# Kernel tuning notes

Hardware: AMD Instinct MI355X
Metric: run time of the kernel (lower is better)

Reference implementation:

```python
import jax, jax.numpy as jnp
import numpy as np

GROUPS = 32
EPS = 1e-5


def setup_inputs() -> dict:
    key = jax.random.key(0)
    ks = jax.random.split(key, 6)
    B, H, W, C = 4, 64, 64, 512
    s = 1.0 / np.sqrt(C)
    return {
        "x": jax.random.normal(ks[0], (B, H, W, C), dtype=jnp.float32),
        "gamma": jnp.ones((C,), jnp.float32),
        "beta": jnp.zeros((C,), jnp.float32),
        "wq": jax.random.normal(ks[1], (C, C), jnp.float32) * s,
        "bq": jnp.zeros((C,), jnp.float32),
        "wk": jax.random.normal(ks[2], (C, C), jnp.float32) * s,
        "bk": jnp.zeros((C,), jnp.float32),
        "wv": jax.random.normal(ks[3], (C, C), jnp.float32) * s,
        "bv": jnp.zeros((C,), jnp.float32),
        "wp": jax.random.normal(ks[4], (C, C), jnp.float32) * s,
        "bp": jnp.zeros((C,), jnp.float32),
    }


def _group_norm(x, gamma, beta):
    B, H, W, C = x.shape
    cg = C // GROUPS
    xg = x.reshape(B, H, W, GROUPS, cg)
    mu = jnp.mean(xg, axis=(1, 2, 4), keepdims=True)
    var = jnp.var(xg, axis=(1, 2, 4), keepdims=True)
    xn = ((xg - mu) * jax.lax.rsqrt(var + EPS)).reshape(B, H, W, C)
    return xn * gamma + beta


def reference(x, gamma, beta, wq, bq, wk, bk, wv, bv, wp, bp):
    B, H, W, C = x.shape
    N = H * W
    xn = _group_norm(x, gamma, beta)
    # 1x1 convs == channel-wise dense layers
    q = (xn @ wq + bq).reshape(B, N, C)
    k = (xn @ wk + bk).reshape(B, N, C)
    v = (xn @ wv + bv).reshape(B, N, C)
    scores = jnp.einsum("bic,bjc->bij", q, k) * (C ** -0.5)  # [B, N, N]
    attn = jax.nn.softmax(scores, axis=-1)
    out = jnp.einsum("bij,bjc->bic", attn, v).reshape(B, H, W, C)
    return out @ wp + bp + x
```

## Files before the change

### kernel.cpp

```cpp
#include <hip/hip_runtime.h>
#include <hip/hip_bf16.h>

typedef __attribute__((ext_vector_type(4))) float f32x4;
typedef __attribute__((ext_vector_type(8))) short s16x8;
typedef unsigned short ushort_t;

#define N_DIM 4096
#define C_DIM 512

static __device__ __forceinline__ unsigned short f2bf(float f) {
    union { float f; unsigned u; } v; v.f = f;
    unsigned r = v.u + 0x7FFFu + ((v.u >> 16) & 1u);
    return (unsigned short)(r >> 16);
}
static __device__ __forceinline__ float bf2f(unsigned short u) {
    union { unsigned u; float f; } v; v.u = ((unsigned)u) << 16;
    return v.f;
}

__global__ void gn_stats_kernel(const float* __restrict__ x, float* __restrict__ stats) {
    int bg = blockIdx.x;
    int b = bg >> 5, g = bg & 31;
    const float* base = x + (size_t)b * (N_DIM * C_DIM) + g * 16;
    float sum = 0.f, ss = 0.f;
    for (int n = threadIdx.x; n < N_DIM; n += 256) {
        const float4* p = (const float4*)(base + (size_t)n * C_DIM);
        #pragma unroll
        for (int t = 0; t < 4; ++t) {
            float4 v = p[t];
            sum += v.x + v.y + v.z + v.w;
            ss  += v.x*v.x + v.y*v.y + v.z*v.z + v.w*v.w;
        }
    }
    #pragma unroll
    for (int o = 32; o > 0; o >>= 1) {
        sum += __shfl_down(sum, o);
        ss  += __shfl_down(ss, o);
    }
    __shared__ float red[8];
    int wid = threadIdx.x >> 6, lane = threadIdx.x & 63;
    if (lane == 0) { red[wid*2] = sum; red[wid*2+1] = ss; }
    __syncthreads();
    if (threadIdx.x == 0) {
        sum = red[0]+red[2]+red[4]+red[6];
        ss  = red[1]+red[3]+red[5]+red[7];
        float mean = sum * (1.f/65536.f);
        float var  = ss  * (1.f/65536.f) - mean*mean;
        stats[bg*2]   = mean;
        stats[bg*2+1] = rsqrtf(var + 1e-5f);
    }
}

__global__ void gn_norm_kernel(const float* __restrict__ x, const float* __restrict__ gamma,
                               const float* __restrict__ beta, const float* __restrict__ stats,
                               ushort_t* __restrict__ xn) {
    size_t i = ((size_t)blockIdx.x * 256 + threadIdx.x) * 4;
    int c = (int)(i & 511);
    int b = (int)(i >> 21);
    int bg = b*32 + (c >> 4);
    float mean = stats[bg*2], rstd = stats[bg*2+1];
    float4 v  = *(const float4*)(x + i);
    float4 ga = *(const float4*)(gamma + c);
    float4 be = *(const float4*)(beta + c);
    ushort4 o;
    o.x = f2bf((v.x - mean) * rstd * ga.x + be.x);
    o.y = f2bf((v.y - mean) * rstd * ga.y + be.y);
    o.z = f2bf((v.z - mean) * rstd * ga.z + be.z);
    o.w = f2bf((v.w - mean) * rstd * ga.w + be.w);
    *(ushort4*)(xn + i) = o;
}

__global__ void wconv_kernel(const float* __restrict__ wq, const float* __restrict__ wk,
                             const float* __restrict__ wv, const float* __restrict__ wp,
                             ushort_t* __restrict__ wt) {
    int idx = blockIdx.x * 256 + threadIdx.x;
    int m = idx >> 18;
    int r = idx & 262143;
    int ci = r >> 9, co = r & 511;
    const float* w = (m == 0) ? wq : (m == 1) ? wk : (m == 2) ? wv : wp;
    wt[(size_t)m * 262144 + (size_t)co * 512 + ci] = f2bf(w[(size_t)ci * 512 + co]);
}

__global__ __launch_bounds__(256) void qkv_kernel(const ushort_t* __restrict__ xn, const ushort_t* __restrict__ wt,
                         const float* __restrict__ bq, const float* __restrict__ bk, const float* __restrict__ bv,
                         ushort_t* __restrict__ q, ushort_t* __restrict__ k, ushort_t* __restrict__ v) {
    __shared__ char alds[2][8192];
    __shared__ char blds[2][8192];
    const int tid = threadIdx.x;
    const int w = tid >> 6, lane = tid & 63;
    const int lr = lane & 15, lg = lane >> 4;
    const int wr = w >> 1, wc = w & 1;
    const int m0 = blockIdx.x * 128;
    const int c0g = blockIdx.y * 128;
    const int z = c0g >> 9;
    const int c0 = c0g & 511;
    const ushort_t* W = wt + (size_t)z * 262144;
    const float* bias = (z == 0) ? bq : (z == 1) ? bk : bv;
    const float scale = (z == 0) ? 0.04419417382415922f : 1.0f;

    f32x4 acc[4][4];
    #pragma unroll
    for (int a = 0; a < 4; ++a)
        #pragma unroll
        for (int b = 0; b < 4; ++b) acc[a][b] = (f32x4){0.f,0.f,0.f,0.f};

    const int g1 = tid, g2 = tid + 256;
    const int r1 = g1 >> 2, s1 = ((g1 & 3) ^ (r1 & 3)) << 4;
    const int r2g = g2 >> 2, s2 = ((g2 & 3) ^ (r2g & 3)) << 4;

    auto STAGE = [&](int buf, int k0) {
        const char* A = (const char*)xn + (size_t)(m0) * 1024 + k0 * 2;
        const char* B = (const char*)W + (size_t)(c0) * 1024 + k0 * 2;
        __builtin_amdgcn_global_load_lds((const __attribute__((address_space(1))) void*)(A + (size_t)r1 * 1024 + s1),
            (__attribute__((address_space(3))) void*)(&alds[buf][g1 * 16]), 16, 0, 0);
        __builtin_amdgcn_global_load_lds((const __attribute__((address_space(1))) void*)(A + (size_t)r2g * 1024 + s2),
            (__attribute__((address_space(3))) void*)(&alds[buf][g2 * 16]), 16, 0, 0);
        __builtin_amdgcn_global_load_lds((const __attribute__((address_space(1))) void*)(B + (size_t)r1 * 1024 + s1),
            (__attribute__((address_space(3))) void*)(&blds[buf][g1 * 16]), 16, 0, 0);
        __builtin_amdgcn_global_load_lds((const __attribute__((address_space(1))) void*)(B + (size_t)r2g * 1024 + s2),
            (__attribute__((address_space(3))) void*)(&blds[buf][g2 * 16]), 16, 0, 0);
    };

    STAGE(0, 0);
    for (int ks = 0; ks < 16; ++ks) {
        const int cur = ks & 1;
        if (ks < 15) {
            STAGE(cur ^ 1, (ks + 1) * 32);
            asm volatile("s_waitcnt vmcnt(4)" ::: "memory");
        } else {
            asm volatile("s_waitcnt vmcnt(0)" ::: "memory");
        }
        __builtin_amdgcn_s_barrier();
        asm volatile("" ::: "memory");
        s16x8 af[4], bf[4];
        #pragma unroll
        for (int mi = 0; mi < 4; ++mi) {
            int row = wr * 64 + mi * 16 + lr;
            af[mi] = *(const s16x8*)(&alds[cur][row * 64 + ((lg ^ (lr & 3)) << 4)]);
        }
        #pragma unroll
        for (int ni = 0; ni < 4; ++ni) {
            int row = wc * 64 + ni * 16 + lr;
            bf[ni] = *(const s16x8*)(&blds[cur][row * 64 + ((lg ^ (lr & 3)) << 4)]);
        }
        #pragma unroll
        for (int mi = 0; mi < 4; ++mi)
            #pragma unroll
            for (int ni = 0; ni < 4; ++ni)
                acc[mi][ni] = __builtin_amdgcn_mfma_f32_16x16x32_bf16(af[mi], bf[ni], acc[mi][ni], 0, 0, 0);
        asm volatile("" ::: "memory");
        __builtin_amdgcn_s_barrier();
    }

    if (z < 2) {
        ushort_t* out = (z == 0) ? q : k;
        #pragma unroll
        for (int ni = 0; ni < 4; ++ni) {
            int cg = c0 + wc * 64 + ni * 16 + lr;
            float bb = bias[cg];
            #pragma unroll
            for (int mi = 0; mi < 4; ++mi) {
                int row = m0 + wr * 64 + mi * 16 + lg * 4;
                #pragma unroll
                for (int r2 = 0; r2 < 4; ++r2)
                    out[(size_t)(row + r2) * 512 + cg] = f2bf((acc[mi][ni][r2] + bb) * scale);
            }
        }
    } else {
        #pragma unroll
        for (int ni = 0; ni < 4; ++ni) {
            int cg = c0 + wc * 64 + ni * 16 + lr;
            float bb = bias[cg];
            #pragma unroll
            for (int mi = 0; mi < 4; ++mi) {
                int row = m0 + wr * 64 + mi * 16 + lg * 4;
                int batch = row >> 12, j = row & 4095;
                ushort4 o;
                o.x = f2bf(acc[mi][ni][0] + bb);
                o.y = f2bf(acc[mi][ni][1] + bb);
                o.z = f2bf(acc[mi][ni][2] + bb);
                o.w = f2bf(acc[mi][ni][3] + bb);
                *(ushort4*)(v + (size_t)batch * (512*4096) + (size_t)cg * 4096 + j) = o;
            }
        }
    }
}

__global__ __launch_bounds__(256) void attn_kernel(const ushort_t* __restrict__ q, const ushort_t* __restrict__ k,
                          const ushort_t* __restrict__ vt, ushort_t* __restrict__ Op0,
                          ushort_t* __restrict__ Op1, float2* __restrict__ stats2) {
    __shared__ char slds[131072 + 8192 + 512];
    char* plds = slds + 131072;
    float* rlds = (float*)(slds + 131072 + 8192);
    const int tid = threadIdx.x;
    const int w = tid >> 6, lane = tid & 63;
    const int lr = lane & 15, lg = lane >> 4;
    const int batch = blockIdx.y;
    const int js = blockIdx.z;
    const int i0 = blockIdx.x * 64;
    const int jbase = js * 2048;
    const char* kb = (const char*)(k  + (size_t)batch * (4096 * 512));
    const char* vb = (const char*)(vt + (size_t)batch * (512 * 4096));
    const ushort_t* qb = q + (size_t)batch * (4096 * 512);

    s16x8 qf[16];
    {
        const ushort_t* qrow = qb + (size_t)(i0 + w * 16 + lr) * 512 + lg * 8;
        #pragma unroll
        for (int t = 0; t < 16; ++t) qf[t] = *(const s16x8*)(qrow + t * 32);
    }

    f32x4 acc[8][4];
    #pragma unroll
    for (int a = 0; a < 8; ++a)
        #pragma unroll
        for (int b = 0; b < 4; ++b) acc[a][b] = (f32x4){0.f,0.f,0.f,0.f};
    float m = -1e30f, s = 0.f;

    const int vswz = ((lane & 3) ^ ((lane >> 3) & 3)) << 4;

    auto STAGE_K = [&](int buf, int j0) {
        char* lb = slds + buf * 65536;
        const char* gk = kb + (size_t)j0 * 1024;
        #pragma unroll
        for (int r = 0; r < 8; ++r) {
            int row = w * 8 + r;
            __builtin_amdgcn_global_load_lds(
                (const __attribute__((address_space(1))) void*)(gk + (size_t)row * 1024 + ((lane ^ r) << 4)),
                (__attribute__((address_space(3))) void*)(lb + row * 1024), 16, 0, 0);
        }
    };
    auto STAGE_V = [&](int buf, int j0) {
        char* lv = slds + buf * 65536 + 32768;
        const char* gv = vb + (size_t)j0 * 2;
        #pragma unroll
        for (int r = 0; r < 8; ++r) {
            int p = w * 8 + r;
            int c = p * 16 + (lane >> 2);
            __builtin_amdgcn_global_load_lds(
                (const __attribute__((address_space(1))) void*)(gv + (size_t)c * 8192 + vswz),
                (__attribute__((address_space(3))) void*)(lv + p * 1024), 16, 0, 0);
        }
    };

    auto QKSM = [&](int buf, int pbuf) {
        const char* kl = slds + buf * 65536;
        f32x4 sa = {0,0,0,0}, sb = {0,0,0,0}, sc2 = {0,0,0,0}, sd = {0,0,0,0};
        #pragma unroll
        for (int tt = 0; tt < 16; tt += 2) {
            s16x8 k0f = *(const s16x8*)(kl + lr * 1024        + ((tt*64 + lg*16)     ^ ((lr&7)*16)));
            s16x8 k1f = *(const s16x8*)(kl + lr * 1024        + (((tt+1)*64 + lg*16) ^ ((lr&7)*16)));
            s16x8 k2f = *(const s16x8*)(kl + (16+lr) * 1024   + ((tt*64 + lg*16)     ^ ((lr&7)*16)));
            s16x8 k3f = *(const s16x8*)(kl + (16+lr) * 1024   + (((tt+1)*64 + lg*16) ^ ((lr&7)*16)));
            sa  = __builtin_amdgcn_mfma_f32_16x16x32_bf16(k0f, qf[tt],   sa,  0,0,0);
            sb  = __builtin_amdgcn_mfma_f32_16x16x32_bf16(k1f, qf[tt+1], sb,  0,0,0);
            sc2 = __builtin_amdgcn_mfma_f32_16x16x32_bf16(k2f, qf[tt],   sc2, 0,0,0);
            sd  = __builtin_amdgcn_mfma_f32_16x16x32_bf16(k3f, qf[tt+1], sd,  0,0,0);
        }
        f32x4 s1 = sa + sb;
        f32x4 s2 = sc2 + sd;

        float tm = fmaxf(fmaxf(fmaxf(s1[0], s1[1]), fmaxf(s1[2], s1[3])),
                         fmaxf(fmaxf(s2[0], s2[1]), fmaxf(s2[2], s2[3])));
        tm = fmaxf(tm, __shfl_xor(tm, 16));
        tm = fmaxf(tm, __shfl_xor(tm, 32));
        float resc = 1.f;
        if (!__all(tm <= m + 8.f)) {
            float mnew = fmaxf(m, tm);
            resc = __expf(m - mnew);
            s *= resc;
            m = mnew;
        }
        f32x4 p1, p2;
        #pragma unroll
        for (int r2 = 0; r2 < 4; ++r2) { p1[r2] = __expf(s1[r2] - m); p2[r2] = __expf(s2[r2] - m); }
        float ts = p1[0]+p1[1]+p1[2]+p1[3] + p2[0]+p2[1]+p2[2]+p2[3];
        ts += __shfl_xor(ts, 16);
        ts += __shfl_xor(ts, 32);
        s += ts;

        unsigned w0 = (unsigned)f2bf(p1[0]) | ((unsigned)f2bf(p1[1]) << 16);
        unsigned w1 = (unsigned)f2bf(p1[2]) | ((unsigned)f2bf(p1[3]) << 16);
        unsigned w2 = (unsigned)f2bf(p2[0]) | ((unsigned)f2bf(p2[1]) << 16);
        unsigned w3 = (unsigned)f2bf(p2[2]) | ((unsigned)f2bf(p2[3]) << 16);
        char* prow = plds + pbuf * 4096 + w * 1024 + lr * 64 + ((lg & 1) << 3);
        *(uint2*)(prow + ((((lg >> 1)    ) ^ (lr & 3)) << 4)) = (uint2){w0, w1};
        *(uint2*)(prow + (((2 | (lg >> 1)) ^ (lr & 3)) << 4)) = (uint2){w2, w3};
        if (lg == 0) rlds[pbuf * 64 + w * 16 + lr] = resc;
    };

    STAGE_K(0, jbase);
    STAGE_V(0, jbase);
    STAGE_K(1, jbase + 32);
    asm volatile("s_waitcnt vmcnt(8)" ::: "memory");
    __builtin_amdgcn_s_barrier();
    asm volatile("" ::: "memory");
    QKSM(0, 0);
    asm volatile("s_waitcnt lgkmcnt(0)" ::: "memory");
    __builtin_amdgcn_s_barrier();
    asm volatile("" ::: "memory");

    for (int t = 0; t < 64; ++t) {
        const int cur = t & 1, nxt = cur ^ 1;
        if (t < 62) STAGE_K(cur, jbase + (t + 2) * 32);
        if (t < 63) STAGE_V(nxt, jbase + (t + 1) * 32);

        {
            const float* rr = rlds + cur * 64;
            float rf0 = rr[lr], rf1 = rr[16 + lr], rf2 = rr[32 + lr], rf3 = rr[48 + lr];
            if (__any(rf0 != 1.f || rf1 != 1.f || rf2 != 1.f || rf3 != 1.f)) {
                #pragma unroll
                for (int ct = 0; ct < 8; ++ct) {
                    acc[ct][0] *= rf0; acc[ct][1] *= rf1; acc[ct][2] *= rf2; acc[ct][3] *= rf3;
                }
            }
        }
        s16x8 pf[4];
        #pragma unroll
        for (int g = 0; g < 4; ++g)
            pf[g] = *(const s16x8*)(plds + cur * 4096 + g * 1024 + lr * 64 + ((lg ^ (lr & 3)) << 4));

        const char* vl = slds + cur * 65536 + 32768;
        #pragma unroll
        for (int ct = 0; ct < 8; ++ct) {
            int c = w * 128 + ct * 16 + lr;
            s16x8 vf = *(const s16x8*)(vl + c * 64 + ((lg ^ ((lr >> 1) & 3)) << 4));
            #pragma unroll
            for (int g = 0; g < 4; ++g)
                acc[ct][g] = __builtin_amdgcn_mfma_f32_16x16x32_bf16(vf, pf[g], acc[ct][g], 0,0,0);
        }

        if (t < 63) QKSM(nxt, nxt);

        asm volatile("s_waitcnt vmcnt(0) lgkmcnt(0)" ::: "memory");
        __builtin_amdgcn_s_barrier();
        asm volatile("" ::: "memory");
    }

    if (lg == 0) {
        rlds[w * 16 + lr] = 1.f / s;
        stats2[((size_t)(batch * 2 + js)) * 4096 + i0 + w * 16 + lr] = (float2){m, s};
    }
    __syncthreads();
    ushort_t* Op = js ? Op1 : Op0;
    float inv0 = rlds[lr], inv1 = rlds[16 + lr], inv2 = rlds[32 + lr], inv3 = rlds[48 + lr];
    #pragma unroll
    for (int ct = 0; ct < 8; ++ct) {
        #pragma unroll
        for (int g = 0; g < 4; ++g) {
            float iv = (g == 0) ? inv0 : (g == 1) ? inv1 : (g == 2) ? inv2 : inv3;
            ushort4 o;
            o.x = f2bf(acc[ct][g][0] * iv);
            o.y = f2bf(acc[ct][g][1] * iv);
            o.z = f2bf(acc[ct][g][2] * iv);
            o.w = f2bf(acc[ct][g][3] * iv);
            *(ushort4*)(Op + ((size_t)batch * 4096 + i0 + g*16 + lr) * 512
                        + w * 128 + ct * 16 + lg * 4) = o;
        }
    }
}

__global__ void combine_kernel(ushort_t* __restrict__ Op0, const ushort_t* __restrict__ Op1,
                               const float2* __restrict__ stats2) {
    int idx = blockIdx.x * 256 + threadIdx.x;
    int row = idx >> 7;
    int cc = (idx & 127) << 2;
    int b = row >> 12, r = row & 4095;
    float2 st0 = stats2[((size_t)(b * 2 + 0)) * 4096 + r];
    float2 st1 = stats2[((size_t)(b * 2 + 1)) * 4096 + r];
    float M = fmaxf(st0.x, st1.x);
    float w0 = __expf(st0.x - M) * st0.y;
    float w1 = __expf(st1.x - M) * st1.y;
    float rden = 1.f / (w0 + w1);
    w0 *= rden; w1 *= rden;
    size_t off = (size_t)row * 512 + cc;
    ushort4 a = *(ushort4*)(Op0 + off);
    ushort4 c4 = *(const ushort4*)(Op1 + off);
    ushort4 o;
    o.x = f2bf(w0 * bf2f(a.x) + w1 * bf2f(c4.x));
    o.y = f2bf(w0 * bf2f(a.y) + w1 * bf2f(c4.y));
    o.z = f2bf(w0 * bf2f(a.z) + w1 * bf2f(c4.z));
    o.w = f2bf(w0 * bf2f(a.w) + w1 * bf2f(c4.w));
    *(ushort4*)(Op0 + off) = o;
}

__global__ __launch_bounds__(256) void proj_kernel(const ushort_t* __restrict__ O, const ushort_t* __restrict__ wt,
                          const float* __restrict__ bp, const float* __restrict__ x, float* __restrict__ out) {
    __shared__ char alds[2][8192];
    __shared__ char blds[2][8192];
    const int tid = threadIdx.x;
    const int w = tid >> 6, lane = tid & 63;
    const int lr = lane & 15, lg = lane >> 4;
    const int wr = w >> 1, wc = w & 1;
    const int m0 = blockIdx.x * 128;
    const int c0 = blockIdx.y * 128;
    const ushort_t* W = wt + (size_t)3 * 262144;

    f32x4 acc[4][4];
    #pragma unroll
    for (int a = 0; a < 4; ++a)
        #pragma unroll
        for (int b = 0; b < 4; ++b) acc[a][b] = (f32x4){0.f,0.f,0.f,0.f};

    const int g1 = tid, g2 = tid + 256;
    const int r1 = g1 >> 2, s1 = ((g1 & 3) ^ (r1 & 3)) << 4;
    const int r2g = g2 >> 2, s2 = ((g2 & 3) ^ (r2g & 3)) << 4;

    auto STAGE = [&](int buf, int k0) {
        const char* A = (const char*)O + (size_t)(m0) * 1024 + k0 * 2;
        const char* B = (const char*)W + (size_t)(c0) * 1024 + k0 * 2;
        __builtin_amdgcn_global_load_lds((const __attribute__((address_space(1))) void*)(A + (size_t)r1 * 1024 + s1),
            (__attribute__((address_space(3))) void*)(&alds[buf][g1 * 16]), 16, 0, 0);
        __builtin_amdgcn_global_load_lds((const __attribute__((address_space(1))) void*)(A + (size_t)r2g * 1024 + s2),
            (__attribute__((address_space(3))) void*)(&alds[buf][g2 * 16]), 16, 0, 0);
        __builtin_amdgcn_global_load_lds((const __attribute__((address_space(1))) void*)(B + (size_t)r1 * 1024 + s1),
            (__attribute__((address_space(3))) void*)(&blds[buf][g1 * 16]), 16, 0, 0);
        __builtin_amdgcn_global_load_lds((const __attribute__((address_space(1))) void*)(B + (size_t)r2g * 1024 + s2),
            (__attribute__((address_space(3))) void*)(&blds[buf][g2 * 16]), 16, 0, 0);
    };

    STAGE(0, 0);
    for (int ks = 0; ks < 16; ++ks) {
        const int cur = ks & 1;
        if (ks < 15) {
            STAGE(cur ^ 1, (ks + 1) * 32);
            asm volatile("s_waitcnt vmcnt(4)" ::: "memory");
        } else {
            asm volatile("s_waitcnt vmcnt(0)" ::: "memory");
        }
        __builtin_amdgcn_s_barrier();
        asm volatile("" ::: "memory");
        s16x8 af[4], bf[4];
        #pragma unroll
        for (int mi = 0; mi < 4; ++mi) {
            int row = wr * 64 + mi * 16 + lr;
            af[mi] = *(const s16x8*)(&alds[cur][row * 64 + ((lg ^ (lr & 3)) << 4)]);
        }
        #pragma unroll
        for (int ni = 0; ni < 4; ++ni) {
            int row = wc * 64 + ni * 16 + lr;
            bf[ni] = *(const s16x8*)(&blds[cur][row * 64 + ((lg ^ (lr & 3)) << 4)]);
        }
        #pragma unroll
        for (int mi = 0; mi < 4; ++mi)
            #pragma unroll
            for (int ni = 0; ni < 4; ++ni)
                acc[mi][ni] = __builtin_amdgcn_mfma_f32_16x16x32_bf16(af[mi], bf[ni], acc[mi][ni], 0, 0, 0);
        asm volatile("" ::: "memory");
        __builtin_amdgcn_s_barrier();
    }

    #pragma unroll
    for (int ni = 0; ni < 4; ++ni) {
        int cg = c0 + wc * 64 + ni * 16 + lr;
        float bb = bp[cg];
        #pragma unroll
        for (int mi = 0; mi < 4; ++mi) {
            int row = m0 + wr * 64 + mi * 16 + lg * 4;
            #pragma unroll
            for (int r2 = 0; r2 < 4; ++r2) {
                size_t idx = (size_t)(row + r2) * 512 + cg;
                out[idx] = acc[mi][ni][r2] + bb + x[idx];
            }
        }
    }
}

extern "C" void kernel_launch(void* const* d_in, const int* in_sizes, int n_in,
                              void* d_out, int out_size, void* d_ws, size_t ws_size,
                              hipStream_t stream) {
    (void)in_sizes; (void)n_in; (void)out_size; (void)ws_size;
    const float* x     = (const float*)d_in[0];
    const float* gamma = (const float*)d_in[1];
    const float* beta  = (const float*)d_in[2];
    const float* wq    = (const float*)d_in[3];
    const float* bq    = (const float*)d_in[4];
    const float* wk    = (const float*)d_in[5];
    const float* bk    = (const float*)d_in[6];
    const float* wv    = (const float*)d_in[7];
    const float* bv    = (const float*)d_in[8];
    const float* wp    = (const float*)d_in[9];
    const float* bp    = (const float*)d_in[10];
    float* out = (float*)d_out;

    char* ws = (char*)d_ws;
    ushort_t* wt    = (ushort_t*)(ws);
    float*    stats = (float*)(ws + (2ull<<20));
    float2*   st2   = (float2*)(ws + (3ull<<20));
    ushort_t* xn    = (ushort_t*)(ws + (4ull<<20));
    ushort_t* qb    = (ushort_t*)(ws + (20ull<<20));
    ushort_t* kb    = (ushort_t*)(ws + (36ull<<20));
    ushort_t* vt    = (ushort_t*)(ws + (52ull<<20));
    ushort_t* Ob    = (ushort_t*)(ws + (68ull<<20));

    hipLaunchKernelGGL(wconv_kernel,    dim3(4096),       dim3(256), 0, stream, wq, wk, wv, wp, wt);
    hipLaunchKernelGGL(gn_stats_kernel, dim3(128),        dim3(256), 0, stream, x, stats);
    hipLaunchKernelGGL(gn_norm_kernel,  dim3(8192),       dim3(256), 0, stream, x, gamma, beta, stats, xn);
    hipLaunchKernelGGL(qkv_kernel,      dim3(128, 12),    dim3(256), 0, stream, xn, wt, bq, bk, bv, qb, kb, vt);
    hipLaunchKernelGGL(attn_kernel,     dim3(64, 4, 2),   dim3(256), 0, stream, qb, kb, vt, Ob, xn, st2);
    hipLaunchKernelGGL(combine_kernel,  dim3(8192),       dim3(256), 0, stream, Ob, xn, st2);
    hipLaunchKernelGGL(proj_kernel,     dim3(128, 4),     dim3(256), 0, stream, Ob, wt, bp, x, out);
}
```

Baseline: 359.1 us.

## Drop split-KV attention and combine kernel; reorder QK softmax ahead of PV

The attention kernel no longer splits the key/value range across two blocks. Each block now walks all 4096 keys, and the separate combine kernel with its partial outputs and per-row stats is removed. This removes an extra launch and the write and re-read of two partial output tensors. The cost is half as many blocks (256 instead of 512), so each block carries a longer serial loop. The next tile's QK/softmax is also moved ahead of the current tile's PV MFMAs to change how instructions interleave, and the prologue wait now drains all outstanding loads.

```diff
diff --git a/kernel.cpp b/kernel.cpp
--- a/kernel.cpp
+++ b/kernel.cpp
@@ -12,10 +12,6 @@
     union { float f; unsigned u; } v; v.f = f;
     unsigned r = v.u + 0x7FFFu + ((v.u >> 16) & 1u);
     return (unsigned short)(r >> 16);
-}
-static __device__ __forceinline__ float bf2f(unsigned short u) {
-    union { unsigned u; float f; } v; v.u = ((unsigned)u) << 16;
-    return v.f;
 }
 
 __global__ void gn_stats_kernel(const float* __restrict__ x, float* __restrict__ stats) {
@@ -187,8 +183,7 @@
 }
 
 __global__ __launch_bounds__(256) void attn_kernel(const ushort_t* __restrict__ q, const ushort_t* __restrict__ k,
-                          const ushort_t* __restrict__ vt, ushort_t* __restrict__ Op0,
-                          ushort_t* __restrict__ Op1, float2* __restrict__ stats2) {
+                          const ushort_t* __restrict__ vt, ushort_t* __restrict__ O) {
     __shared__ char slds[131072 + 8192 + 512];
     char* plds = slds + 131072;
     float* rlds = (float*)(slds + 131072 + 8192);
@@ -196,9 +191,7 @@
     const int w = tid >> 6, lane = tid & 63;
     const int lr = lane & 15, lg = lane >> 4;
     const int batch = blockIdx.y;
-    const int js = blockIdx.z;
     const int i0 = blockIdx.x * 64;
-    const int jbase = js * 2048;
     const char* kb = (const char*)(k  + (size_t)batch * (4096 * 512));
     const char* vb = (const char*)(vt + (size_t)batch * (512 * 4096));
     const ushort_t* qb = q + (size_t)batch * (4096 * 512);
@@ -289,10 +282,10 @@
         if (lg == 0) rlds[pbuf * 64 + w * 16 + lr] = resc;
     };
 
-    STAGE_K(0, jbase);
-    STAGE_V(0, jbase);
-    STAGE_K(1, jbase + 32);
-    asm volatile("s_waitcnt vmcnt(8)" ::: "memory");
+    STAGE_K(0, 0);
+    STAGE_V(0, 0);
+    STAGE_K(1, 32);
+    asm volatile("s_waitcnt vmcnt(0)" ::: "memory");
     __builtin_amdgcn_s_barrier();
     asm volatile("" ::: "memory");
     QKSM(0, 0);
@@ -300,10 +293,12 @@
     __builtin_amdgcn_s_barrier();
     asm volatile("" ::: "memory");
 
-    for (int t = 0; t < 64; ++t) {
+    for (int t = 0; t < 128; ++t) {
         const int cur = t & 1, nxt = cur ^ 1;
-        if (t < 62) STAGE_K(cur, jbase + (t + 2) * 32);
-        if (t < 63) STAGE_V(nxt, jbase + (t + 1) * 32);
+        if (t < 126) STAGE_K(cur, (t + 2) * 32);
+        if (t < 127) STAGE_V(nxt, (t + 1) * 32);
+
+        if (t < 127) QKSM(nxt, nxt);
 
         {
             const float* rr = rlds + cur * 64;
@@ -330,19 +325,13 @@
                 acc[ct][g] = __builtin_amdgcn_mfma_f32_16x16x32_bf16(vf, pf[g], acc[ct][g], 0,0,0);
         }
 
-        if (t < 63) QKSM(nxt, nxt);
-
         asm volatile("s_waitcnt vmcnt(0) lgkmcnt(0)" ::: "memory");
         __builtin_amdgcn_s_barrier();
         asm volatile("" ::: "memory");
     }
 
-    if (lg == 0) {
-        rlds[w * 16 + lr] = 1.f / s;
-        stats2[((size_t)(batch * 2 + js)) * 4096 + i0 + w * 16 + lr] = (float2){m, s};
-    }
+    if (lg == 0) rlds[w * 16 + lr] = 1.f / s;
     __syncthreads();
-    ushort_t* Op = js ? Op1 : Op0;
     float inv0 = rlds[lr], inv1 = rlds[16 + lr], inv2 = rlds[32 + lr], inv3 = rlds[48 + lr];
     #pragma unroll
     for (int ct = 0; ct < 8; ++ct) {
@@ -354,34 +343,10 @@
             o.y = f2bf(acc[ct][g][1] * iv);
             o.z = f2bf(acc[ct][g][2] * iv);
             o.w = f2bf(acc[ct][g][3] * iv);
-            *(ushort4*)(Op + ((size_t)batch * 4096 + i0 + g*16 + lr) * 512
+            *(ushort4*)(O + ((size_t)batch * 4096 + i0 + g*16 + lr) * 512
                         + w * 128 + ct * 16 + lg * 4) = o;
         }
     }
-}
-
-__global__ void combine_kernel(ushort_t* __restrict__ Op0, const ushort_t* __restrict__ Op1,
-                               const float2* __restrict__ stats2) {
-    int idx = blockIdx.x * 256 + threadIdx.x;
-    int row = idx >> 7;
-    int cc = (idx & 127) << 2;
-    int b = row >> 12, r = row & 4095;
-    float2 st0 = stats2[((size_t)(b * 2 + 0)) * 4096 + r];
-    float2 st1 = stats2[((size_t)(b * 2 + 1)) * 4096 + r];
-    float M = fmaxf(st0.x, st1.x);
-    float w0 = __expf(st0.x - M) * st0.y;
-    float w1 = __expf(st1.x - M) * st1.y;
-    float rden = 1.f / (w0 + w1);
-    w0 *= rden; w1 *= rden;
-    size_t off = (size_t)row * 512 + cc;
-    ushort4 a = *(ushort4*)(Op0 + off);
-    ushort4 c4 = *(const ushort4*)(Op1 + off);
-    ushort4 o;
-    o.x = f2bf(w0 * bf2f(a.x) + w1 * bf2f(c4.x));
-    o.y = f2bf(w0 * bf2f(a.y) + w1 * bf2f(c4.y));
-    o.z = f2bf(w0 * bf2f(a.z) + w1 * bf2f(c4.z));
-    o.w = f2bf(w0 * bf2f(a.w) + w1 * bf2f(c4.w));
-    *(ushort4*)(Op0 + off) = o;
 }
 
 __global__ __launch_bounds__(256) void proj_kernel(const ushort_t* __restrict__ O, const ushort_t* __restrict__ wt,
@@ -486,7 +451,6 @@
     char* ws = (char*)d_ws;
     ushort_t* wt    = (ushort_t*)(ws);
     float*    stats = (float*)(ws + (2ull<<20));
-    float2*   st2   = (float2*)(ws + (3ull<<20));
     ushort_t* xn    = (ushort_t*)(ws + (4ull<<20));
     ushort_t* qb    = (ushort_t*)(ws + (20ull<<20));
     ushort_t* kb    = (ushort_t*)(ws + (36ull<<20));
@@ -497,7 +461,6 @@
     hipLaunchKernelGGL(gn_stats_kernel, dim3(128),        dim3(256), 0, stream, x, stats);
     hipLaunchKernelGGL(gn_norm_kernel,  dim3(8192),       dim3(256), 0, stream, x, gamma, beta, stats, xn);
     hipLaunchKernelGGL(qkv_kernel,      dim3(128, 12),    dim3(256), 0, stream, xn, wt, bq, bk, bv, qb, kb, vt);
-    hipLaunchKernelGGL(attn_kernel,     dim3(64, 4, 2),   dim3(256), 0, stream, qb, kb, vt, Ob, xn, st2);
-    hipLaunchKernelGGL(combine_kernel,  dim3(8192),       dim3(256), 0, stream, Ob, xn, st2);
+    hipLaunchKernelGGL(attn_kernel,     dim3(64, 4),      dim3(256), 0, stream, qb, kb, vt, Ob);
     hipLaunchKernelGGL(proj_kernel,     dim3(128, 4),     dim3(256), 0, stream, Ob, wt, bp, x, out);
 }
```

Result: faster. 341.4 us (-4.9%).
